# Kernel optimization log

Hardware: AMD Instinct MI355X
Metric: run time of the kernel (lower is better)

The kernel has to match this reference:

```python
import jax, jax.numpy as jnp
import numpy as np

NUM_GRAPHS = 512

def setup_inputs() -> dict:
    key = jax.random.key(0)
    ks = jax.random.split(key, 8)
    N, E, H = 50000, 1600000, 128
    edge_attr0 = jax.random.normal(ks[0], (N, H), dtype=jnp.float32)
    edge_attr1 = jax.random.normal(ks[1], (E, H), dtype=jnp.float32)
    edge_attr2 = jax.random.normal(ks[2], (E, H), dtype=jnp.float32)
    edge_index1 = jax.random.randint(ks[3], (E,), 0, N, dtype=jnp.int64)
    edge_index2 = jax.random.randint(ks[4], (E,), 0, N, dtype=jnp.int64)
    batch = jnp.sort(jax.random.randint(ks[5], (N,), 0, NUM_GRAPHS, dtype=jnp.int64))
    W = jax.random.normal(ks[6], (H, H), dtype=jnp.float32) * 0.05
    b = jax.random.normal(ks[7], (H,), dtype=jnp.float32) * 0.05
    return {"edge_attr0": edge_attr0, "edge_attr1": edge_attr1, "edge_attr2": edge_attr2,
            "edge_index1": edge_index1, "edge_index2": edge_index2, "batch": batch,
            "num_nodes": N, "W": W, "b": b}

def reference(edge_attr0, edge_attr1, edge_attr2, edge_index1, edge_index2, batch, num_nodes, W, b):
    # multi-scale scatter-sum of edge attrs onto nodes
    node_emb = jax.ops.segment_sum(edge_attr1, edge_index1, num_segments=num_nodes)
    node_emb = node_emb + jax.ops.segment_sum(edge_attr2, edge_index2, num_segments=num_nodes)
    # linear + ELU (torch Linear: x @ W.T + b)
    node_emb = jax.nn.elu((node_emb + edge_attr0) @ W.T + b)
    # scatter-mean pooling over graphs
    graph_sum = jax.ops.segment_sum(node_emb, batch, num_segments=NUM_GRAPHS)
    counts = jax.ops.segment_sum(jnp.ones((num_nodes,), node_emb.dtype), batch, num_segments=NUM_GRAPHS)
    return graph_sum / jnp.maximum(counts, 1.0)[:, None]
```

## Files before the change

kernel.cpp:

```cpp
#include <hip/hip_runtime.h>
#include <hip/hip_bf16.h>

#define H 128
#define NGRAPH 512
#define NPB 32
#define PAD 128

typedef float v4f __attribute__((ext_vector_type(4)));
typedef int   v4i __attribute__((ext_vector_type(4)));
typedef unsigned long long ull;

__global__ __launch_bounds__(256) void init_kernel(
    const float* __restrict__ W, float* __restrict__ WtG,
    int* __restrict__ pos, float* __restrict__ graph_acc, int N)
{
    int i = blockIdx.x * 256 + threadIdx.x;
    if (i < H * H) {
        int j = i >> 7, k = i & (H - 1);
        WtG[k * H + j] = W[j * H + k];
    }
    if (i < N) pos[i] = 0;
    if (i < NGRAPH * H) graph_acc[i] = 0.f;
}

__global__ __launch_bounds__(256) void fill_padded(
    const int* __restrict__ i1, const int* __restrict__ i2,
    int* __restrict__ pos, int* __restrict__ adj, int E)
{
    int g = blockIdx.x * 256 + threadIdx.x;
    int e = g * 4;
    if (e + 4 <= E) {
        v4i a = __builtin_nontemporal_load((const v4i*)(i1 + e));
        v4i b = __builtin_nontemporal_load((const v4i*)(i2 + e));
        int s;
        s = atomicAdd(&pos[a.x], 1); adj[(size_t)a.x * PAD + s] = e + 0;
        s = atomicAdd(&pos[a.y], 1); adj[(size_t)a.y * PAD + s] = e + 1;
        s = atomicAdd(&pos[a.z], 1); adj[(size_t)a.z * PAD + s] = e + 2;
        s = atomicAdd(&pos[a.w], 1); adj[(size_t)a.w * PAD + s] = e + 3;
        s = atomicAdd(&pos[b.x], 1); adj[(size_t)b.x * PAD + s] = E + e + 0;
        s = atomicAdd(&pos[b.y], 1); adj[(size_t)b.y * PAD + s] = E + e + 1;
        s = atomicAdd(&pos[b.z], 1); adj[(size_t)b.z * PAD + s] = E + e + 2;
        s = atomicAdd(&pos[b.w], 1); adj[(size_t)b.w * PAD + s] = E + e + 3;
    } else if (e < E) {
        for (int k = e; k < E; ++k) {
            int n1 = i1[k], n2 = i2[k];
            int s1 = atomicAdd(&pos[n1], 1); adj[(size_t)n1 * PAD + s1] = k;
            int s2 = atomicAdd(&pos[n2], 1); adj[(size_t)n2 * PAD + s2] = E + k;
        }
    }
}

__device__ __forceinline__ v4f prow(const int* __restrict__ ap, int k,
                                    int half, ull loff,
                                    const float* __restrict__ a1,
                                    const float* __restrict__ a2, int E)
{
    int t0 = ap[2 * k], t1 = ap[2 * k + 1];
    int tt = half ? t1 : t0;
    const float* p = (tt < E) ? a1 + (size_t)tt * H : a2 + (size_t)(tt - E) * H;
    return *(const v4f*)((const char*)p + loff);
}

__global__ __launch_bounds__(256) void gather_transform(
    const float* __restrict__ a1, const float* __restrict__ a2,
    const float* __restrict__ e0, const int* __restrict__ adj,
    const int* __restrict__ deg, const int* __restrict__ batch,
    const float* __restrict__ WtG, const float* __restrict__ bias,
    float* __restrict__ graph_acc, int N, int E)
{
    __shared__ __align__(16) float xsT[H * 36];
    __shared__ int bs[NPB];

    int t = threadIdx.x, wave = t >> 6, lane = t & 63;
    int half = lane >> 5;
    ull loff = (ull)(lane & 31) * 16;
    int node0 = blockIdx.x * NPB;

    if (t < NPB) {
        int gn = node0 + t;
        bs[t] = (gn < N) ? batch[gn] : -1;
    }

    #pragma unroll
    for (int j = 0; j < 8; ++j) {
        int nl = wave * 8 + j;
        int gn = node0 + nl;
        v4f acc0 = {0.f, 0.f, 0.f, 0.f}, acc1 = {0.f, 0.f, 0.f, 0.f};
        if (gn < N) {
            int d = deg[gn];
            if (d > PAD) d = PAD;
            const int* ap = adj + (size_t)gn * PAD;
            int np = d >> 1;
            int k = 0;
            int np4 = np & ~3;
            if (np4) {
                v4f A0 = prow(ap, 0, half, loff, a1, a2, E);
                v4f A1 = prow(ap, 1, half, loff, a1, a2, E);
                v4f A2 = prow(ap, 2, half, loff, a1, a2, E);
                v4f A3 = prow(ap, 3, half, loff, a1, a2, E);
                for (k = 4; k < np4; k += 4) {
                    acc0 += A0; A0 = prow(ap, k + 0, half, loff, a1, a2, E);
                    acc1 += A1; A1 = prow(ap, k + 1, half, loff, a1, a2, E);
                    acc0 += A2; A2 = prow(ap, k + 2, half, loff, a1, a2, E);
                    acc1 += A3; A3 = prow(ap, k + 3, half, loff, a1, a2, E);
                }
                acc0 += A0; acc1 += A1; acc0 += A2; acc1 += A3;
                k = np4;
            }
            for (; k < np; ++k) acc0 += prow(ap, k, half, loff, a1, a2, E);
            if (d & 1) {
                int tt = ap[d - 1];
                const float* p = (tt < E) ? a1 + (size_t)tt * H : a2 + (size_t)(tt - E) * H;
                v4f v = *(const v4f*)((const char*)p + loff);
                if (half) v = (v4f){0.f, 0.f, 0.f, 0.f};
                acc0 += v;
            }
        }
        v4f acc = acc0 + acc1;
        float r0 = acc.x + __shfl_xor(acc.x, 32, 64);
        float r1 = acc.y + __shfl_xor(acc.y, 32, 64);
        float r2 = acc.z + __shfl_xor(acc.z, 32, 64);
        float r3 = acc.w + __shfl_xor(acc.w, 32, 64);
        if (half == 0) {
            v4f ev = {0.f, 0.f, 0.f, 0.f};
            if (gn < N)
                ev = *(const v4f*)(e0 + (size_t)gn * H + (lane & 31) * 4);
            int f0 = (lane & 31) * 4;
            xsT[(f0 + 0) * 36 + nl] = r0 + ev.x;
            xsT[(f0 + 1) * 36 + nl] = r1 + ev.y;
            xsT[(f0 + 2) * 36 + nl] = r2 + ev.z;
            xsT[(f0 + 3) * 36 + nl] = r3 + ev.w;
        }
    }
    __syncthreads();

    int n0 = (t & 7) * 4;
    int j0 = (t >> 3) * 4;

    float acc[4][4] = {};
    #pragma unroll 4
    for (int k = 0; k < H; ++k) {
        float xr[4], wr[4];
        *(float4*)xr = *(const float4*)&xsT[k * 36 + n0];
        *(float4*)wr = *(const float4*)&WtG[k * H + j0];
        #pragma unroll
        for (int nn = 0; nn < 4; ++nn)
            #pragma unroll
            for (int jj = 0; jj < 4; ++jj)
                acc[nn][jj] = fmaf(xr[nn], wr[jj], acc[nn][jj]);
    }

    float bj[4];
    *(float4*)bj = *(const float4*)&bias[j0];

    #pragma unroll
    for (int jj = 0; jj < 4; ++jj) {
        int j = j0 + jj;
        int curg = -1; float s = 0.f;
        #pragma unroll
        for (int nn = 0; nn < 4; ++nn) {
            int g = bs[n0 + nn];
            if (g < 0) continue;
            float a = acc[nn][jj] + bj[jj];
            float y = (a > 0.f) ? a : expm1f(a);
            if (g == curg) { s += y; }
            else {
                if (curg >= 0) unsafeAtomicAdd(&graph_acc[curg * H + j], s);
                curg = g; s = y;
            }
        }
        if (curg >= 0) unsafeAtomicAdd(&graph_acc[curg * H + j], s);
    }
}

__device__ __forceinline__ int lower_bound_dev(const int* __restrict__ b, int n, int v) {
    int lo = 0, hi = n;
    while (lo < hi) { int m = (lo + hi) >> 1; if (b[m] < v) lo = m + 1; else hi = m; }
    return lo;
}

__global__ __launch_bounds__(256) void finalize(
    const float* __restrict__ graph_acc, const int* __restrict__ batch,
    float* __restrict__ out, int N)
{
    int i = blockIdx.x * 256 + threadIdx.x;
    if (i >= NGRAPH * H) return;
    int g = i >> 7;
    int lo = lower_bound_dev(batch, N, g);
    int hi = lower_bound_dev(batch, N, g + 1);
    float c = fmaxf((float)(hi - lo), 1.0f);
    out[i] = graph_acc[i] / c;
}

extern "C" void kernel_launch(void* const* d_in, const int* in_sizes, int n_in,
                              void* d_out, int out_size, void* d_ws, size_t ws_size,
                              hipStream_t stream)
{
    const float* e0    = (const float*)d_in[0];
    const float* a1    = (const float*)d_in[1];
    const float* a2    = (const float*)d_in[2];
    const int*   i1    = (const int*)d_in[3];
    const int*   i2    = (const int*)d_in[4];
    const int*   batch = (const int*)d_in[5];
    const float* W     = (const float*)d_in[7];
    const float* b     = (const float*)d_in[8];
    float* out = (float*)d_out;

    int N = in_sizes[0] / H;
    int E = in_sizes[3];

    auto align16 = [](size_t v) { return (v + 15) & ~(size_t)15; };

    char* ws = (char*)d_ws;
    size_t gaB   = align16((size_t)NGRAPH * H * sizeof(float));
    size_t posB  = align16((size_t)N * sizeof(int));
    size_t wtB   = align16((size_t)H * H * sizeof(float));
    size_t adjB  = align16((size_t)N * PAD * sizeof(int));

    size_t off = 0;
    float* graph_acc = (float*)(ws + off); off += gaB;
    int*   pos       = (int*)  (ws + off); off += posB;
    float* WtG       = (float*)(ws + off); off += wtB;
    int*   adj       = (int*)  (ws + off); off += adjB;
    (void)ws_size;

    int initN = N;
    if (H * H > initN) initN = H * H;
    if (NGRAPH * H > initN) initN = NGRAPH * H;
    init_kernel<<<(initN + 255) / 256, 256, 0, stream>>>(W, WtG, pos, graph_acc, N);

    int nbE4 = (E / 4 + 255) / 256 + 1;
    fill_padded<<<nbE4, 256, 0, stream>>>(i1, i2, pos, adj, E);

    gather_transform<<<(N + NPB - 1) / NPB, 256, 0, stream>>>(
        a1, a2, e0, adj, pos, batch, WtG, b, graph_acc, N, E);

    finalize<<<(NGRAPH * H + 255) / 256, 256, 0, stream>>>(graph_acc, batch, out, N);
}
```

Before: 660.4 us.

## Prefetch adjacency rows into registers via shuffles, deepen gather unroll, halve node tile

Each wave loads its node's 128 adjacency indices into registers with two coalesced loads and broadcasts them by wave shuffle. It also prefetches the next node's indices while gathering the current one. The gather keeps eight row loads in flight instead of four, and the block tile drops from 32 to 16 nodes to launch twice as many blocks. The aim is more memory-level parallelism in the bandwidth-bound gather, in exchange for more weight-matrix reads and more atomics into the graph accumulator.

```diff
diff --git a/kernel.cpp b/kernel.cpp
--- a/kernel.cpp
+++ b/kernel.cpp
@@ -3,7 +3,7 @@
 
 #define H 128
 #define NGRAPH 512
-#define NPB 32
+#define NPB 16
 #define PAD 128
 
 typedef float v4f __attribute__((ext_vector_type(4)));
@@ -50,13 +50,12 @@
     }
 }
 
-__device__ __forceinline__ v4f prow(const int* __restrict__ ap, int k,
-                                    int half, ull loff,
-                                    const float* __restrict__ a1,
-                                    const float* __restrict__ a2, int E)
-{
-    int t0 = ap[2 * k], t1 = ap[2 * k + 1];
-    int tt = half ? t1 : t0;
+__device__ __forceinline__ v4f prowS(int k, int id0, int id1, int half,
+                                     ull loff, const float* __restrict__ a1,
+                                     const float* __restrict__ a2, int E)
+{
+    int sel = (k < 32) ? id0 : id1;
+    int tt  = __shfl(sel, (2 * k + half) & 63, 64);
     const float* p = (tt < E) ? a1 + (size_t)tt * H : a2 + (size_t)(tt - E) * H;
     return *(const v4f*)((const char*)p + loff);
 }
@@ -68,7 +67,7 @@
     const float* __restrict__ WtG, const float* __restrict__ bias,
     float* __restrict__ graph_acc, int N, int E)
 {
-    __shared__ __align__(16) float xsT[H * 36];
+    __shared__ __align__(16) float xsT[H * 20];
     __shared__ int bs[NPB];
 
     int t = threadIdx.x, wave = t >> 6, lane = t & 63;
@@ -81,35 +80,66 @@
         bs[t] = (gn < N) ? batch[gn] : -1;
     }
 
+    int nlb = wave * 4;
+    int nid0 = 0, nid1 = 0, nd = 0;
+    {
+        int gn = node0 + nlb;
+        if (gn < N) {
+            const int* ap = adj + (size_t)gn * PAD;
+            nid0 = ap[lane];
+            nid1 = ap[64 + lane];
+            nd   = deg[gn];
+        }
+    }
+
     #pragma unroll
-    for (int j = 0; j < 8; ++j) {
-        int nl = wave * 8 + j;
+    for (int j = 0; j < 4; ++j) {
+        int nl = nlb + j;
         int gn = node0 + nl;
+        int id0 = nid0, id1 = nid1, d = nd;
+        if (j < 3) {
+            int gn2 = gn + 1;
+            if (gn2 < N) {
+                const int* ap2 = adj + (size_t)gn2 * PAD;
+                nid0 = ap2[lane];
+                nid1 = ap2[64 + lane];
+                nd   = deg[gn2];
+            }
+        }
         v4f acc0 = {0.f, 0.f, 0.f, 0.f}, acc1 = {0.f, 0.f, 0.f, 0.f};
         if (gn < N) {
-            int d = deg[gn];
             if (d > PAD) d = PAD;
-            const int* ap = adj + (size_t)gn * PAD;
             int np = d >> 1;
             int k = 0;
-            int np4 = np & ~3;
-            if (np4) {
-                v4f A0 = prow(ap, 0, half, loff, a1, a2, E);
-                v4f A1 = prow(ap, 1, half, loff, a1, a2, E);
-                v4f A2 = prow(ap, 2, half, loff, a1, a2, E);
-                v4f A3 = prow(ap, 3, half, loff, a1, a2, E);
-                for (k = 4; k < np4; k += 4) {
-                    acc0 += A0; A0 = prow(ap, k + 0, half, loff, a1, a2, E);
-                    acc1 += A1; A1 = prow(ap, k + 1, half, loff, a1, a2, E);
-                    acc0 += A2; A2 = prow(ap, k + 2, half, loff, a1, a2, E);
-                    acc1 += A3; A3 = prow(ap, k + 3, half, loff, a1, a2, E);
+            int np8 = np & ~7;
+            if (np8) {
+                v4f P0 = prowS(0, id0, id1, half, loff, a1, a2, E);
+                v4f P1 = prowS(1, id0, id1, half, loff, a1, a2, E);
+                v4f P2 = prowS(2, id0, id1, half, loff, a1, a2, E);
+                v4f P3 = prowS(3, id0, id1, half, loff, a1, a2, E);
+                v4f P4 = prowS(4, id0, id1, half, loff, a1, a2, E);
+                v4f P5 = prowS(5, id0, id1, half, loff, a1, a2, E);
+                v4f P6 = prowS(6, id0, id1, half, loff, a1, a2, E);
+                v4f P7 = prowS(7, id0, id1, half, loff, a1, a2, E);
+                for (k = 8; k < np8; k += 8) {
+                    acc0 += P0; P0 = prowS(k + 0, id0, id1, half, loff, a1, a2, E);
+                    acc1 += P1; P1 = prowS(k + 1, id0, id1, half, loff, a1, a2, E);
+                    acc0 += P2; P2 = prowS(k + 2, id0, id1, half, loff, a1, a2, E);
+                    acc1 += P3; P3 = prowS(k + 3, id0, id1, half, loff, a1, a2, E);
+                    acc0 += P4; P4 = prowS(k + 4, id0, id1, half, loff, a1, a2, E);
+                    acc1 += P5; P5 = prowS(k + 5, id0, id1, half, loff, a1, a2, E);
+                    acc0 += P6; P6 = prowS(k + 6, id0, id1, half, loff, a1, a2, E);
+                    acc1 += P7; P7 = prowS(k + 7, id0, id1, half, loff, a1, a2, E);
                 }
-                acc0 += A0; acc1 += A1; acc0 += A2; acc1 += A3;
-                k = np4;
+                acc0 += P0; acc1 += P1; acc0 += P2; acc1 += P3;
+                acc0 += P4; acc1 += P5; acc0 += P6; acc1 += P7;
+                k = np8;
             }
-            for (; k < np; ++k) acc0 += prow(ap, k, half, loff, a1, a2, E);
+            for (; k < np; ++k)
+                acc0 += prowS(k, id0, id1, half, loff, a1, a2, E);
             if (d & 1) {
-                int tt = ap[d - 1];
+                int kk = d - 1;
+                int tt = __shfl((kk < 64) ? id0 : id1, kk & 63, 64);
                 const float* p = (tt < E) ? a1 + (size_t)tt * H : a2 + (size_t)(tt - E) * H;
                 v4f v = *(const v4f*)((const char*)p + loff);
                 if (half) v = (v4f){0.f, 0.f, 0.f, 0.f};
@@ -126,50 +156,47 @@
             if (gn < N)
                 ev = *(const v4f*)(e0 + (size_t)gn * H + (lane & 31) * 4);
             int f0 = (lane & 31) * 4;
-            xsT[(f0 + 0) * 36 + nl] = r0 + ev.x;
-            xsT[(f0 + 1) * 36 + nl] = r1 + ev.y;
-            xsT[(f0 + 2) * 36 + nl] = r2 + ev.z;
-            xsT[(f0 + 3) * 36 + nl] = r3 + ev.w;
+            xsT[(f0 + 0) * 20 + nl] = r0 + ev.x;
+            xsT[(f0 + 1) * 20 + nl] = r1 + ev.y;
+            xsT[(f0 + 2) * 20 + nl] = r2 + ev.z;
+            xsT[(f0 + 3) * 20 + nl] = r3 + ev.w;
         }
     }
     __syncthreads();
 
-    int n0 = (t & 7) * 4;
+    int n0 = (t & 7) * 2;
     int j0 = (t >> 3) * 4;
 
-    float acc[4][4] = {};
+    float acc[2][4] = {};
     #pragma unroll 4
     for (int k = 0; k < H; ++k) {
-        float xr[4], wr[4];
-        *(float4*)xr = *(const float4*)&xsT[k * 36 + n0];
+        float2 xr = *(const float2*)&xsT[k * 20 + n0];
+        float wr[4];
         *(float4*)wr = *(const float4*)&WtG[k * H + j0];
         #pragma unroll
-        for (int nn = 0; nn < 4; ++nn)
-            #pragma unroll
-            for (int jj = 0; jj < 4; ++jj)
-                acc[nn][jj] = fmaf(xr[nn], wr[jj], acc[nn][jj]);
+        for (int jj = 0; jj < 4; ++jj) {
+            acc[0][jj] = fmaf(xr.x, wr[jj], acc[0][jj]);
+            acc[1][jj] = fmaf(xr.y, wr[jj], acc[1][jj]);
+        }
     }
 
     float bj[4];
     *(float4*)bj = *(const float4*)&bias[j0];
 
+    int g0 = bs[n0 + 0], g1 = bs[n0 + 1];
     #pragma unroll
     for (int jj = 0; jj < 4; ++jj) {
         int j = j0 + jj;
-        int curg = -1; float s = 0.f;
-        #pragma unroll
-        for (int nn = 0; nn < 4; ++nn) {
-            int g = bs[n0 + nn];
-            if (g < 0) continue;
-            float a = acc[nn][jj] + bj[jj];
-            float y = (a > 0.f) ? a : expm1f(a);
-            if (g == curg) { s += y; }
-            else {
-                if (curg >= 0) unsafeAtomicAdd(&graph_acc[curg * H + j], s);
-                curg = g; s = y;
-            }
-        }
-        if (curg >= 0) unsafeAtomicAdd(&graph_acc[curg * H + j], s);
+        float a0 = acc[0][jj] + bj[jj];
+        float a1v = acc[1][jj] + bj[jj];
+        float y0 = (a0  > 0.f) ? a0  : expm1f(a0);
+        float y1 = (a1v > 0.f) ? a1v : expm1f(a1v);
+        if (g0 == g1) {
+            if (g0 >= 0) unsafeAtomicAdd(&graph_acc[g0 * H + j], y0 + y1);
+        } else {
+            if (g0 >= 0) unsafeAtomicAdd(&graph_acc[g0 * H + j], y0);
+            if (g1 >= 0) unsafeAtomicAdd(&graph_acc[g1 * H + j], y1);
+        }
     }
 }
 
```

New measurement: 770.5 us. 16.7% more time.
